# Kernel tuning notes

Measured on AMD Instinct MI355X. Metric: run time of the kernel, lower is better.

Reference implementation:

```python
import jax, jax.numpy as jnp
import numpy as np
import math

N = 100000   # nodes
E = 500000   # edges
IN_C = 128
EDGE_D = 64
HEADS = 4
OUT_C = 32
HC = HEADS * OUT_C  # 128


def setup_inputs() -> dict:
    key = jax.random.key(0)
    ks = jax.random.split(key, 12)
    s_in = 1.0 / math.sqrt(IN_C)
    s_e = 1.0 / math.sqrt(EDGE_D)
    return {
        "x": jax.random.normal(ks[0], (N, IN_C), jnp.float32),
        "edge_index": jax.random.randint(ks[1], (2, E), 0, N, dtype=jnp.int32),
        "edge_attr": jax.random.normal(ks[2], (E, EDGE_D), jnp.float32),
        "Wq": jax.random.uniform(ks[3], (HC, IN_C), jnp.float32, -s_in, s_in),
        "bq": jax.random.uniform(ks[4], (HC,), jnp.float32, -s_in, s_in),
        "Wk": jax.random.uniform(ks[5], (HC, IN_C), jnp.float32, -s_in, s_in),
        "bk": jax.random.uniform(ks[6], (HC,), jnp.float32, -s_in, s_in),
        "Wv": jax.random.uniform(ks[7], (HC, IN_C), jnp.float32, -s_in, s_in),
        "bv": jax.random.uniform(ks[8], (HC,), jnp.float32, -s_in, s_in),
        "We": jax.random.uniform(ks[9], (HC, EDGE_D), jnp.float32, -s_e, s_e),
        "Ws": jax.random.uniform(ks[10], (HC, IN_C), jnp.float32, -s_in, s_in),
        "bs": jax.random.uniform(ks[11], (HC,), jnp.float32, -s_in, s_in),
    }


def reference(x, edge_index, edge_attr, Wq, bq, Wk, bk, Wv, bv, We, Ws, bs):
    src = edge_index[0]
    dst = edge_index[1]
    x_i = x[dst]                       # [E, IN_C] target-node feats
    x_j = x[src]                       # [E, IN_C] source-node feats

    e = (edge_attr @ We.T).reshape(E, HEADS, OUT_C)
    q = (x_i @ Wq.T + bq).reshape(E, HEADS, OUT_C)
    k = (x_j @ Wk.T + bk).reshape(E, HEADS, OUT_C) + e

    alpha = jnp.sum(q * k, axis=-1) / jnp.sqrt(jnp.float32(OUT_C))  # [E, H]
    # Faithful to the source: GLOBAL per-column max (not per-segment), then
    # segment-sum of exponentials over destination nodes.
    m = jnp.max(alpha, axis=0)                                      # [H]
    exp_a = jnp.exp(alpha - m)                                      # [E, H]
    denom = jax.ops.segment_sum(exp_a, dst, num_segments=N)         # [N, H]
    alpha = exp_a / (denom[dst] + 1e-16)                            # [E, H]

    v = (x_j @ Wv.T + bv).reshape(E, HEADS, OUT_C) + e
    msg = v * alpha[:, :, None]                                     # [E, H, C]

    out = jax.ops.segment_sum(msg.reshape(E, HC), dst, num_segments=N)  # [N, HC]
    out = out + (x @ Ws.T + bs)
    return out
```

## Files before the change

kernel.cpp:

```cpp
#include <hip/hip_runtime.h>
#include <hip/hip_bf16.h>
#include <math.h>

#define N_NODES 100000
#define N_EDGES 500000
#define M0 8.0f
#define INV_SQRT32 0.17677669529663687f

#define NB_PROJ 1563
#define NB_EE   3907
#define GRID_MEGA (NB_PROJ + NB_EE)

typedef __attribute__((ext_vector_type(8))) short bf16x8;
typedef __attribute__((ext_vector_type(4))) float f32x4;
typedef __attribute__((ext_vector_type(8))) unsigned short us8;

static __device__ __forceinline__ unsigned short f2bf(float f) {
    __hip_bfloat16 h = __float2bfloat16(f);
    return *(unsigned short*)&h;
}

static __device__ __forceinline__ void split4(float4 v, ushort4& hv, ushort4& lv) {
    const unsigned short h0 = f2bf(v.x), h1 = f2bf(v.y),
                         h2 = f2bf(v.z), h3 = f2bf(v.w);
    hv.x = h0; hv.y = h1; hv.z = h2; hv.w = h3;
    lv.x = f2bf(v.x - __uint_as_float((unsigned)h0 << 16));
    lv.y = f2bf(v.y - __uint_as_float((unsigned)h1 << 16));
    lv.z = f2bf(v.z - __uint_as_float((unsigned)h2 << 16));
    lv.w = f2bf(v.w - __uint_as_float((unsigned)h3 << 16));
}

static __device__ __forceinline__ void gl_lds16(
    const unsigned short* __restrict__ g, unsigned short* l)
{
    __builtin_amdgcn_global_load_lds(
        (const __attribute__((address_space(1))) unsigned int*)g,
        (__attribute__((address_space(3))) unsigned int*)l, 16, 0, 0);
}

__global__ __launch_bounds__(256) void prep_kernel(
    const float* __restrict__ Wq, const float* __restrict__ Wk,
    const float* __restrict__ Wv, const float* __restrict__ Ws,
    const float* __restrict__ We,
    unsigned short* __restrict__ WBh, unsigned short* __restrict__ WBl,
    unsigned short* __restrict__ WEh, unsigned short* __restrict__ WEl,
    int* __restrict__ cursor)
{
    const int i = blockIdx.x * 256 + threadIdx.x;
    if (i < N_NODES) cursor[i] = 0;
    if (i < 65536) {
        const int p = i >> 14;
        const float* W = (p == 0) ? Wq : (p == 1) ? Wk : (p == 2) ? Wv : Ws;
        const float v = W[i & 16383];
        const unsigned short h = f2bf(v);
        WBh[i] = h;
        WBl[i] = f2bf(v - __uint_as_float((unsigned)h << 16));
    } else if (i < 73728) {
        const int idx = i - 65536;
        const float v = We[idx];
        const unsigned short h = f2bf(v);
        WEh[idx] = h;
        WEl[idx] = f2bf(v - __uint_as_float((unsigned)h << 16));
    }
}

__global__ __launch_bounds__(512, 4) void mega_kernel(
    const float* __restrict__ x, const int* __restrict__ ei,
    const float* __restrict__ ea,
    const unsigned short* __restrict__ WBh, const unsigned short* __restrict__ WBl,
    const unsigned short* __restrict__ WEh, const unsigned short* __restrict__ WEl,
    const float* __restrict__ bq, const float* __restrict__ bk,
    const float* __restrict__ bv, const float* __restrict__ bs,
    float* __restrict__ Qn, float* __restrict__ Kn, float* __restrict__ Vn,
    float* __restrict__ out, unsigned short* __restrict__ Ee,
    int* __restrict__ cursor)
{
    __shared__ __align__(16) unsigned short sAh[8192];
    __shared__ __align__(16) unsigned short sAl[8192];
    __shared__ __align__(16) unsigned short sWh[8192];
    __shared__ __align__(16) unsigned short sWl[8192];

    const int t = threadIdx.x;
    const int bid = blockIdx.x;

    const int lane = t & 63;
    const int wid = t >> 6;
    const int fr = lane & 15;
    const int fq = lane >> 4;

    if (bid < NB_PROJ) {
        const long r0 = (long)bid * 64;

        for (int i = t; i < 2048; i += 512) {
            const int r = i >> 5;
            const int k4 = (i & 31) * 4;
            const long row = r0 + r;
            float4 v = (row < N_NODES) ? *(const float4*)&x[row * 128 + k4]
                                       : make_float4(0.f, 0.f, 0.f, 0.f);
            ushort4 hv, lv; split4(v, hv, lv);
            const int di = r * 128 + (k4 ^ ((r & 7) << 3));
            *(ushort4*)&sAh[di] = hv;
            *(ushort4*)&sAl[di] = lv;
        }

        for (int p = 0; p < 4; ++p) {
            const float* bias = (p == 0) ? bq : (p == 1) ? bk : (p == 2) ? bv : bs;
            float* dst        = (p == 0) ? Qn : (p == 1) ? Kn : (p == 2) ? Vn : out;

            f32x4 acc[4];
#pragma unroll
            for (int m = 0; m < 4; ++m) acc[m] = (f32x4){0.f, 0.f, 0.f, 0.f};

            for (int kc = 0; kc < 2; ++kc) {
                __syncthreads();
#pragma unroll
                for (int c = 0; c < 2; ++c) {
                    const int i = c * 512 + t;
                    const int r = i >> 3;
                    const int d = i & 7;
                    const int gi = p * 16384 + r * 128 + kc * 64 + ((d ^ (r & 7)) * 8);
                    gl_lds16(&WBh[gi], &sWh[i * 8]);
                    gl_lds16(&WBl[gi], &sWl[i * 8]);
                }
                __syncthreads();

#pragma unroll
                for (int ks = 0; ks < 2; ++ks) {
                    const int kx = kc * 64 + ks * 32 + fq * 8;
                    const int kw = ks * 32 + fq * 8;
                    bf16x8 ah[4], al[4], wh, wl;
#pragma unroll
                    for (int m = 0; m < 4; ++m) {
                        const int r = m * 16 + fr;
                        const int di = r * 128 + (kx ^ ((r & 7) << 3));
                        ah[m] = *(const bf16x8*)&sAh[di];
                        al[m] = *(const bf16x8*)&sAl[di];
                    }
                    {
                        const int r = wid * 16 + fr;
                        const int di = r * 64 + (kw ^ ((r & 7) << 3));
                        wh = *(const bf16x8*)&sWh[di];
                        wl = *(const bf16x8*)&sWl[di];
                    }
#pragma unroll
                    for (int m = 0; m < 4; ++m) {
                        acc[m] = __builtin_amdgcn_mfma_f32_16x16x32_bf16(
                            ah[m], wh, acc[m], 0, 0, 0);
                        acc[m] = __builtin_amdgcn_mfma_f32_16x16x32_bf16(
                            ah[m], wl, acc[m], 0, 0, 0);
                        acc[m] = __builtin_amdgcn_mfma_f32_16x16x32_bf16(
                            al[m], wh, acc[m], 0, 0, 0);
                    }
                }
            }

            const float bb = bias[wid * 16 + fr];
#pragma unroll
            for (int m = 0; m < 4; ++m) {
                const long rowb = r0 + m * 16 + fq * 4;
#pragma unroll
                for (int j = 0; j < 4; ++j) {
                    if (rowb + j < N_NODES)
                        dst[(rowb + j) * 128 + wid * 16 + fr] = acc[m][j] + bb;
                }
            }
        }
    } else {
        const long e0 = (long)(bid - NB_PROJ) * 128;
        const int wr = wid >> 2;
        const int wc = wid & 3;

        if (t < 128) {
            const long e = e0 + t;
            if (e < N_EDGES) atomicAdd(&cursor[ei[N_EDGES + e]], 1);
        }

#pragma unroll
        for (int c = 0; c < 2; ++c) {
            const int i = c * 512 + t;
            const int r = i >> 3;
            const int d = i & 7;
            const int gi = r * 64 + ((d ^ (r & 7)) * 8);
            gl_lds16(&WEh[gi], &sWh[i * 8]);
            gl_lds16(&WEl[gi], &sWl[i * 8]);
        }
        for (int i = t; i < 2048; i += 512) {
            const int r = i >> 4;
            const int k4 = (i & 15) * 4;
            const long e = e0 + r;
            float4 v = (e < N_EDGES) ? *(const float4*)&ea[e * 64 + k4]
                                     : make_float4(0.f, 0.f, 0.f, 0.f);
            ushort4 hv, lv; split4(v, hv, lv);
            const int di = r * 64 + (k4 ^ ((r & 7) << 3));
            *(ushort4*)&sAh[di] = hv;
            *(ushort4*)&sAl[di] = lv;
        }
        __syncthreads();

        f32x4 acc[4][2];
#pragma unroll
        for (int m = 0; m < 4; ++m)
#pragma unroll
            for (int n = 0; n < 2; ++n) acc[m][n] = (f32x4){0.f, 0.f, 0.f, 0.f};

#pragma unroll
        for (int ks = 0; ks < 2; ++ks) {
            const int kk = ks * 32 + fq * 8;
            bf16x8 ah[4], al[4], wh[2], wl[2];
#pragma unroll
            for (int m = 0; m < 4; ++m) {
                const int r = wr * 64 + m * 16 + fr;
                const int di = r * 64 + (kk ^ ((r & 7) << 3));
                ah[m] = *(const bf16x8*)&sAh[di];
                al[m] = *(const bf16x8*)&sAl[di];
            }
#pragma unroll
            for (int n = 0; n < 2; ++n) {
                const int r = wc * 32 + n * 16 + fr;
                const int di = r * 64 + (kk ^ ((r & 7) << 3));
                wh[n] = *(const bf16x8*)&sWh[di];
                wl[n] = *(const bf16x8*)&sWl[di];
            }
#pragma unroll
            for (int m = 0; m < 4; ++m)
#pragma unroll
                for (int n = 0; n < 2; ++n) {
                    acc[m][n] = __builtin_amdgcn_mfma_f32_16x16x32_bf16(
                        ah[m], wh[n], acc[m][n], 0, 0, 0);
                    acc[m][n] = __builtin_amdgcn_mfma_f32_16x16x32_bf16(
                        ah[m], wl[n], acc[m][n], 0, 0, 0);
                    acc[m][n] = __builtin_amdgcn_mfma_f32_16x16x32_bf16(
                        al[m], wh[n], acc[m][n], 0, 0, 0);
                }
        }

#pragma unroll
        for (int m = 0; m < 4; ++m) {
            const long e = e0 + wr * 64 + m * 16 + fq * 4;
#pragma unroll
            for (int j = 0; j < 4; ++j) {
                if (e + j < N_EDGES) {
#pragma unroll
                    for (int n = 0; n < 2; ++n)
                        Ee[(e + j) * 128 + wc * 32 + n * 16 + fr] =
                            f2bf(acc[m][n][j]);
                }
            }
        }
    }
}

__global__ __launch_bounds__(1024) void csr_scan_kernel(
    int* __restrict__ cursor, int* __restrict__ csr_off)
{
    __shared__ int wsum[16];
    const int t = threadIdx.x;
    const int lane = t & 63;
    const int wid = t >> 6;
    const int n0 = t * 100;
    const bool active = (t < 1000);

    int tsum = 0;
    if (active) {
        for (int q = 0; q < 25; ++q) {
            const int4 d = *(const int4*)&cursor[n0 + q * 4];
            tsum += d.x + d.y + d.z + d.w;
        }
    }
    int inc = tsum;
#pragma unroll
    for (int o = 1; o < 64; o <<= 1) {
        const int v = __shfl_up(inc, o, 64);
        if (lane >= o) inc += v;
    }
    if (lane == 63) wsum[wid] = inc;
    __syncthreads();
    if (t == 0) {
        int run = 0;
#pragma unroll
        for (int w = 0; w < 16; ++w) { const int v = wsum[w]; wsum[w] = run; run += v; }
        csr_off[N_NODES] = run;
    }
    __syncthreads();
    if (active) {
        int run = wsum[wid] + inc - tsum;
        for (int q = 0; q < 25; ++q) {
            const int n = n0 + q * 4;
            const int4 d = *(const int4*)&cursor[n];
            int4 offv;
            offv.x = run; run += d.x;
            offv.y = run; run += d.y;
            offv.z = run; run += d.z;
            offv.w = run; run += d.w;
            *(int4*)&csr_off[n] = offv;
            *(int4*)&cursor[n]  = offv;
        }
    }
}

__global__ __launch_bounds__(256) void csr_fill_kernel(
    const int* __restrict__ ei, int* __restrict__ cursor,
    int2* __restrict__ csr_es)
{
    const int e = blockIdx.x * 256 + threadIdx.x;
    if (e >= N_EDGES) return;
    const int dst = ei[N_EDGES + e];
    const int pos = atomicAdd(&cursor[dst], 1);
    csr_es[pos] = make_int2(e, ei[e]);
}

__global__ __launch_bounds__(256) void fused_attn_kernel(
    const int* __restrict__ csr_off, const int2* __restrict__ csr_es,
    const unsigned short* __restrict__ Ee,
    const float* __restrict__ Qn, const float* __restrict__ Kn,
    const float* __restrict__ Vn, float* __restrict__ out)
{
    const int lane = threadIdx.x & 63;
    const int l2 = lane * 2;
    const long n = (long)blockIdx.x * 4 + (threadIdx.x >> 6);

    const int off0 = csr_off[n];
    const int off1 = csr_off[n + 1];
    const float2 q = *(const float2*)&Qn[n * 128 + l2];

    float dsum = 0.f;
    float2 acc = make_float2(0.f, 0.f);
    for (int base = off0; base < off1; base += 64) {
        const int cnt = min(64, off1 - base);
        int2 es = make_int2(0, 0);
        if (base + lane < off1) es = csr_es[base + lane];
        for (int j = 0; j < cnt; ++j) {
            const long e = __shfl(es.x, j, 64);
            const long s = __shfl(es.y, j, 64);
            const unsigned u = *(const unsigned*)&Ee[e * 128 + l2];
            const float2 k = *(const float2*)&Kn[s * 128 + l2];
            const float ea0 = __uint_as_float(u << 16);
            const float ea1 = __uint_as_float(u & 0xffff0000u);
            float p = q.x * (k.x + ea0) + q.y * (k.y + ea1);
#pragma unroll
            for (int o = 1; o < 16; o <<= 1) p += __shfl_xor(p, o, 64);
            const float an = __expf(p * INV_SQRT32 - M0);
            dsum += an;
            const float2 v = *(const float2*)&Vn[s * 128 + l2];
            acc.x = fmaf(v.x + ea0, an, acc.x);
            acc.y = fmaf(v.y + ea1, an, acc.y);
        }
    }
    const float rd = 1.f / (dsum + 1e-16f);
    float2 o = *(const float2*)&out[n * 128 + l2];
    o.x = fmaf(acc.x, rd, o.x);
    o.y = fmaf(acc.y, rd, o.y);
    *(float2*)&out[n * 128 + l2] = o;
}

extern "C" void kernel_launch(void* const* d_in, const int* in_sizes, int n_in,
                              void* d_out, int out_size, void* d_ws, size_t ws_size,
                              hipStream_t stream)
{
    const float* x  = (const float*)d_in[0];
    const int*   ei = (const int*)d_in[1];
    const float* ea = (const float*)d_in[2];
    const float* Wq = (const float*)d_in[3];
    const float* bq = (const float*)d_in[4];
    const float* Wk = (const float*)d_in[5];
    const float* bk = (const float*)d_in[6];
    const float* Wv = (const float*)d_in[7];
    const float* bv = (const float*)d_in[8];
    const float* We = (const float*)d_in[9];
    const float* Ws = (const float*)d_in[10];
    const float* bs = (const float*)d_in[11];
    float* out = (float*)d_out;

    float* ws = (float*)d_ws;
    float* Qn = ws;
    float* Kn = ws + 12800000;
    float* Vn = ws + 25600000;
    int* csr_off = (int*)(ws + 38400000);
    int* cursor  = (int*)(ws + 38500004);
    int2* csr_es = (int2*)(ws + 38600004);
    unsigned short* WBh = (unsigned short*)(ws + 40000000);
    unsigned short* WBl = (unsigned short*)(ws + 40050000);
    unsigned short* WEh = (unsigned short*)(ws + 40100000);
    unsigned short* WEl = (unsigned short*)(ws + 40110000);
    unsigned short* Ee = (unsigned short*)((char*)d_ws + 163200032);

    prep_kernel<<<391, 256, 0, stream>>>(Wq, Wk, Wv, Ws, We,
                                         WBh, WBl, WEh, WEl, cursor);

    mega_kernel<<<GRID_MEGA, 512, 0, stream>>>(x, ei, ea,
                                               WBh, WBl, WEh, WEl,
                                               bq, bk, bv, bs,
                                               Qn, Kn, Vn, out, Ee, cursor);

    csr_scan_kernel<<<1, 1024, 0, stream>>>(cursor, csr_off);

    csr_fill_kernel<<<(N_EDGES + 255) / 256, 256, 0, stream>>>(ei, cursor, csr_es);

    fused_attn_kernel<<<25000, 256, 0, stream>>>(csr_off, csr_es, Ee,
                                                 Qn, Kn, Vn, out);
}
```

Before: 551.4 us.

## Load weights directly from global into registers and unroll edge gather loop by two

The projection and edge-embedding GEMM branches now read weight fragments straight from global memory (L2/L1-resident) into registers instead of staging them through LDS with global_load_lds and barriers. This removes the weight LDS buffers and the per-chunk __syncthreads, shrinking LDS use and possibly raising occupancy. Separately, the per-node aggregation loop processes two edges per iteration so more gathers are in flight at once. The trade-off is uncoalesced, redundant global weight reads per wave and more registers in the aggregation loop.

```diff
diff --git a/kernel.cpp b/kernel.cpp
--- a/kernel.cpp
+++ b/kernel.cpp
@@ -13,7 +13,6 @@
 
 typedef __attribute__((ext_vector_type(8))) short bf16x8;
 typedef __attribute__((ext_vector_type(4))) float f32x4;
-typedef __attribute__((ext_vector_type(8))) unsigned short us8;
 
 static __device__ __forceinline__ unsigned short f2bf(float f) {
     __hip_bfloat16 h = __float2bfloat16(f);
@@ -28,14 +27,6 @@
     lv.y = f2bf(v.y - __uint_as_float((unsigned)h1 << 16));
     lv.z = f2bf(v.z - __uint_as_float((unsigned)h2 << 16));
     lv.w = f2bf(v.w - __uint_as_float((unsigned)h3 << 16));
-}
-
-static __device__ __forceinline__ void gl_lds16(
-    const unsigned short* __restrict__ g, unsigned short* l)
-{
-    __builtin_amdgcn_global_load_lds(
-        (const __attribute__((address_space(1))) unsigned int*)g,
-        (__attribute__((address_space(3))) unsigned int*)l, 16, 0, 0);
 }
 
 __global__ __launch_bounds__(256) void prep_kernel(
@@ -77,8 +68,6 @@
 {
     __shared__ __align__(16) unsigned short sAh[8192];
     __shared__ __align__(16) unsigned short sAl[8192];
-    __shared__ __align__(16) unsigned short sWh[8192];
-    __shared__ __align__(16) unsigned short sWl[8192];
 
     const int t = threadIdx.x;
     const int bid = blockIdx.x;
@@ -102,45 +91,33 @@
             *(ushort4*)&sAh[di] = hv;
             *(ushort4*)&sAl[di] = lv;
         }
+        __syncthreads();
 
         for (int p = 0; p < 4; ++p) {
             const float* bias = (p == 0) ? bq : (p == 1) ? bk : (p == 2) ? bv : bs;
             float* dst        = (p == 0) ? Qn : (p == 1) ? Kn : (p == 2) ? Vn : out;
 
+            const unsigned short* Wh = WBh + p * 16384 + (wid * 16 + fr) * 128;
+            const unsigned short* Wl = WBl + p * 16384 + (wid * 16 + fr) * 128;
+
             f32x4 acc[4];
 #pragma unroll
             for (int m = 0; m < 4; ++m) acc[m] = (f32x4){0.f, 0.f, 0.f, 0.f};
 
+#pragma unroll
             for (int kc = 0; kc < 2; ++kc) {
-                __syncthreads();
-#pragma unroll
-                for (int c = 0; c < 2; ++c) {
-                    const int i = c * 512 + t;
-                    const int r = i >> 3;
-                    const int d = i & 7;
-                    const int gi = p * 16384 + r * 128 + kc * 64 + ((d ^ (r & 7)) * 8);
-                    gl_lds16(&WBh[gi], &sWh[i * 8]);
-                    gl_lds16(&WBl[gi], &sWl[i * 8]);
-                }
-                __syncthreads();
-
 #pragma unroll
                 for (int ks = 0; ks < 2; ++ks) {
                     const int kx = kc * 64 + ks * 32 + fq * 8;
-                    const int kw = ks * 32 + fq * 8;
-                    bf16x8 ah[4], al[4], wh, wl;
+                    const bf16x8 wh = *(const bf16x8*)&Wh[kx];
+                    const bf16x8 wl = *(const bf16x8*)&Wl[kx];
+                    bf16x8 ah[4], al[4];
 #pragma unroll
                     for (int m = 0; m < 4; ++m) {
                         const int r = m * 16 + fr;
                         const int di = r * 128 + (kx ^ ((r & 7) << 3));
                         ah[m] = *(const bf16x8*)&sAh[di];
                         al[m] = *(const bf16x8*)&sAl[di];
-                    }
-                    {
-                        const int r = wid * 16 + fr;
-                        const int di = r * 64 + (kw ^ ((r & 7) << 3));
-                        wh = *(const bf16x8*)&sWh[di];
-                        wl = *(const bf16x8*)&sWl[di];
                     }
 #pragma unroll
                     for (int m = 0; m < 4; ++m) {
@@ -175,15 +152,6 @@
             if (e < N_EDGES) atomicAdd(&cursor[ei[N_EDGES + e]], 1);
         }
 
-#pragma unroll
-        for (int c = 0; c < 2; ++c) {
-            const int i = c * 512 + t;
-            const int r = i >> 3;
-            const int d = i & 7;
-            const int gi = r * 64 + ((d ^ (r & 7)) * 8);
-            gl_lds16(&WEh[gi], &sWh[i * 8]);
-            gl_lds16(&WEl[gi], &sWl[i * 8]);
-        }
         for (int i = t; i < 2048; i += 512) {
             const int r = i >> 4;
             const int k4 = (i & 15) * 4;
@@ -216,10 +184,9 @@
             }
 #pragma unroll
             for (int n = 0; n < 2; ++n) {
-                const int r = wc * 32 + n * 16 + fr;
-                const int di = r * 64 + (kk ^ ((r & 7) << 3));
-                wh[n] = *(const bf16x8*)&sWh[di];
-                wl[n] = *(const bf16x8*)&sWl[di];
+                const int gi = (wc * 32 + n * 16 + fr) * 64 + kk;
+                wh[n] = *(const bf16x8*)&WEh[gi];
+                wl[n] = *(const bf16x8*)&WEl[gi];
             }
 #pragma unroll
             for (int m = 0; m < 4; ++m)
@@ -329,21 +296,39 @@
         const int cnt = min(64, off1 - base);
         int2 es = make_int2(0, 0);
         if (base + lane < off1) es = csr_es[base + lane];
-        for (int j = 0; j < cnt; ++j) {
-            const long e = __shfl(es.x, j, 64);
-            const long s = __shfl(es.y, j, 64);
-            const unsigned u = *(const unsigned*)&Ee[e * 128 + l2];
-            const float2 k = *(const float2*)&Kn[s * 128 + l2];
-            const float ea0 = __uint_as_float(u << 16);
-            const float ea1 = __uint_as_float(u & 0xffff0000u);
-            float p = q.x * (k.x + ea0) + q.y * (k.y + ea1);
-#pragma unroll
-            for (int o = 1; o < 16; o <<= 1) p += __shfl_xor(p, o, 64);
-            const float an = __expf(p * INV_SQRT32 - M0);
-            dsum += an;
-            const float2 v = *(const float2*)&Vn[s * 128 + l2];
-            acc.x = fmaf(v.x + ea0, an, acc.x);
-            acc.y = fmaf(v.y + ea1, an, acc.y);
+        for (int j = 0; j < cnt; j += 2) {
+            const int j1 = (j + 1 < cnt) ? j + 1 : j;
+            const long eA = __shfl(es.x, j, 64);
+            const long sA = __shfl(es.y, j, 64);
+            const long eB = __shfl(es.x, j1, 64);
+            const long sB = __shfl(es.y, j1, 64);
+            const unsigned ua = *(const unsigned*)&Ee[eA * 128 + l2];
+            const float2 ka = *(const float2*)&Kn[sA * 128 + l2];
+            const float2 va = *(const float2*)&Vn[sA * 128 + l2];
+            const unsigned ub = *(const unsigned*)&Ee[eB * 128 + l2];
+            const float2 kb = *(const float2*)&Kn[sB * 128 + l2];
+            const float2 vb = *(const float2*)&Vn[sB * 128 + l2];
+            const float a0 = __uint_as_float(ua << 16);
+            const float a1 = __uint_as_float(ua & 0xffff0000u);
+            const float b0 = __uint_as_float(ub << 16);
+            const float b1 = __uint_as_float(ub & 0xffff0000u);
+            float pa = q.x * (ka.x + a0) + q.y * (ka.y + a1);
+            float pb = q.x * (kb.x + b0) + q.y * (kb.y + b1);
+#pragma unroll
+            for (int o = 1; o < 16; o <<= 1) {
+                pa += __shfl_xor(pa, o, 64);
+                pb += __shfl_xor(pb, o, 64);
+            }
+            const float ana = __expf(pa * INV_SQRT32 - M0);
+            dsum += ana;
+            acc.x = fmaf(va.x + a0, ana, acc.x);
+            acc.y = fmaf(va.y + a1, ana, acc.y);
+            if (j + 1 < cnt) {
+                const float anb = __expf(pb * INV_SQRT32 - M0);
+                dsum += anb;
+                acc.x = fmaf(vb.x + b0, anb, acc.x);
+                acc.y = fmaf(vb.y + b1, anb, acc.y);
+            }
         }
     }
     const float rd = 1.f / (dsum + 1e-16f);
```

Measured after the change: 676.2 us. 1.23x slower.
